# Kernel tuning notes

Measured on AMD Instinct MI355X. Metric: run time of the kernel, lower is better.

Reference implementation:

```python
import jax, jax.numpy as jnp
import numpy as np
from jax import lax

NUM_TAGS = 48
BATCH = 512
SEQ_LEN = 1024


def setup_inputs() -> dict:
    key = jax.random.key(0)
    k1, k2, k3, k4 = jax.random.split(key, 4)
    emissions = jax.random.normal(k1, (BATCH, SEQ_LEN, NUM_TAGS), dtype=jnp.float32)
    mask = jnp.ones((BATCH, SEQ_LEN), dtype=jnp.int32)
    transitions = jax.random.normal(k2, (NUM_TAGS, NUM_TAGS), dtype=jnp.float32)
    start_transitions = jax.random.normal(k3, (NUM_TAGS,), dtype=jnp.float32)
    end_transitions = jax.random.normal(k4, (NUM_TAGS,), dtype=jnp.float32)
    return {
        "emissions": emissions,
        "mask": mask,
        "transitions": transitions,
        "start_transitions": start_transitions,
        "end_transitions": end_transitions,
    }


def reference(emissions, mask, transitions, start_transitions, end_transitions):
    """Viterbi decode. mask is accepted but unused, matching the original module."""
    # emissions: [B, S, T]
    init_scores = start_transitions + emissions[:, 0]  # [B, T]

    def step(scores, em_t):
        # scores: [B, T] best score ending in each prev tag
        scores_with_trans = scores[:, :, None] + transitions  # [B, Tprev, Tcur]
        idx = jnp.argmax(scores_with_trans, axis=1)            # [B, T] backpointers
        new_scores = jnp.max(scores_with_trans, axis=1) + em_t  # [B, T]
        return new_scores, idx

    # scan over timesteps 1..S-1 (time-major emissions)
    em_rest = jnp.swapaxes(emissions[:, 1:], 0, 1)  # [S-1, B, T]
    scores, backptrs = lax.scan(step, init_scores, em_rest)  # backptrs: [S-1, B, T]

    scores = scores + end_transitions
    best_tags = jnp.argmax(scores, axis=1)  # [B] tag at position S-1

    def backtrace(tag, bp_t):
        # tag: [B] tag at position t+1; bp_t: [B, T] backpointers into position t
        prev = jnp.take_along_axis(bp_t, tag[:, None], axis=1)[:, 0]
        return prev, tag  # emit tag at position t+1

    first_tag, tags_rest = lax.scan(backtrace, best_tags, backptrs, reverse=True)
    # tags_rest[i] = tag at position i+1, shape [S-1, B]
    best_paths = jnp.concatenate(
        [first_tag[:, None], jnp.swapaxes(tags_rest, 0, 1)], axis=1
    )  # [B, S]
    return best_paths
```

## Files before the change

kernel.cpp:

```cpp
#include <hip/hip_runtime.h>

#define NTAG 48
#define SEQ 1024
#define NBATCH 512

__device__ __forceinline__ float rl_f32(float v, int lane) {
    return __int_as_float(__builtin_amdgcn_readlane(__float_as_int(v), lane));
}

__device__ __forceinline__ float max3(float a, float b, float c) {
    float d;
    asm("v_max3_f32 %0, %1, %2, %3" : "=v"(d) : "v"(a), "v"(b), "v"(c));
    return d;
}

__global__ __launch_bounds__(64, 1) void crf_viterbi_kernel(
    const float* __restrict__ em,
    const float* __restrict__ trans,
    const float* __restrict__ start,
    const float* __restrict__ endt,
    int* __restrict__ out,
    unsigned char* __restrict__ bp)
{
    const int b  = blockIdx.x;
    const int j  = threadIdx.x;
    const int jj = (j < NTAG) ? j : (NTAG - 1);

    __shared__ int obuf[SEQ];

    float trg[NTAG];
#pragma unroll
    for (int i = 0; i < NTAG; ++i) trg[i] = trans[i * NTAG + jj];

    const float* emb = em + (size_t)b * SEQ * NTAG;
    unsigned char* bpb = bp + (size_t)b * SEQ * NTAG;

    float score = start[jj] + emb[jj];

    float em_p1 = emb[1 * NTAG + jj];
    float em_p2 = emb[2 * NTAG + jj];

    for (int t = 1; t < SEQ; ++t) {
        float em_j = em_p1;
        em_p1 = em_p2;
        int tn = (t + 2 < SEQ) ? (t + 2) : (SEQ - 1);
        em_p2 = emb[tn * NTAG + jj];

        float cand[NTAG];
#pragma unroll
        for (int i = 0; i < NTAG; ++i)
            cand[i] = rl_f32(score, i) + trg[i];

        float l1[16];
#pragma unroll
        for (int k = 0; k < 16; ++k)
            l1[k] = max3(cand[3 * k], cand[3 * k + 1], cand[3 * k + 2]);
        float l2[6];
#pragma unroll
        for (int k = 0; k < 5; ++k)
            l2[k] = max3(l1[3 * k], l1[3 * k + 1], l1[3 * k + 2]);
        l2[5] = l1[15];
        float m0 = max3(l2[0], l2[1], l2[2]);
        float m1 = max3(l2[3], l2[4], l2[5]);
        float best = fmaxf(m0, m1);

        int pi = 0;
#pragma unroll
        for (int i = NTAG - 1; i >= 0; --i)
            pi = (cand[i] == best) ? i : pi;

        if (j < NTAG) bpb[(size_t)t * NTAG + j] = (unsigned char)pi;
        score = best + em_j;
    }

    score += endt[jj];

    float m = rl_f32(score, 0); int tag = 0;
#pragma unroll
    for (int i = 1; i < NTAG; ++i) {
        float v = rl_f32(score, i);
        if (v > m) { m = v; tag = i; }
    }

    if (j == 0) obuf[SEQ - 1] = tag;

    int cur[16], nxt[16];
    int t = SEQ - 1;
    int n = 16;
#pragma unroll
    for (int k = 0; k < 16; ++k)
        cur[k] = (int)bpb[(size_t)(t - k) * NTAG + jj];

    while (t >= 1) {
        int t2 = t - n;
        int n2 = 0;
        if (t2 >= 1) {
            n2 = (t2 >= 16) ? 16 : t2;
#pragma unroll
            for (int k = 0; k < 16; ++k)
                if (k < n2) nxt[k] = (int)bpb[(size_t)(t2 - k) * NTAG + jj];
        }
#pragma unroll
        for (int k = 0; k < 16; ++k) {
            if (k < n) {
                tag = __shfl(cur[k], tag, 64);
                if (j == 0) obuf[t - k - 1] = tag;
            }
        }
#pragma unroll
        for (int k = 0; k < 16; ++k) cur[k] = nxt[k];
        t = t2; n = n2;
    }

    __syncthreads();

    int* outb = out + (size_t)b * SEQ;
#pragma unroll
    for (int t0 = 0; t0 < SEQ / 64; ++t0)
        outb[t0 * 64 + j] = obuf[t0 * 64 + j];
}

extern "C" void kernel_launch(void* const* d_in, const int* in_sizes, int n_in,
                              void* d_out, int out_size, void* d_ws, size_t ws_size,
                              hipStream_t stream) {
    const float* em    = (const float*)d_in[0];
    const float* trans = (const float*)d_in[2];
    const float* start = (const float*)d_in[3];
    const float* endt  = (const float*)d_in[4];
    int* out = (int*)d_out;
    unsigned char* bpw = (unsigned char*)d_ws;

    crf_viterbi_kernel<<<NBATCH, 64, 0, stream>>>(em, trans, start, endt, out, bpw);
}
```

Baseline: 920.5 us.

## Store forward scores and recompute backpointers during backtrace instead of storing argmax

The forward Viterbi loop no longer computes or stores per-step argmax backpointers. Instead it writes each step's score row to workspace as floats. The backtrace recomputes the argmax from the stored scores plus a transposed transition matrix in LDS, using a wave max reduction and ballot. This removes the 48 compare/select ops per step from the serial forward chain. In exchange it quadruples workspace traffic and lengthens each serial backtrace step with several dependent shuffles.

Result: slower. 973.4 us (+5.7%).

```diff
diff --git a/kernel.cpp b/kernel.cpp
--- a/kernel.cpp
+++ b/kernel.cpp
@@ -3,6 +3,7 @@
 #define NTAG 48
 #define SEQ 1024
 #define NBATCH 512
+#define NEG_INF (-3.402823466e+38f)
 
 __device__ __forceinline__ float rl_f32(float v, int lane) {
     return __int_as_float(__builtin_amdgcn_readlane(__float_as_int(v), lane));
@@ -20,22 +21,33 @@
     const float* __restrict__ start,
     const float* __restrict__ endt,
     int* __restrict__ out,
-    unsigned char* __restrict__ bp)
+    float* __restrict__ srows)
 {
     const int b  = blockIdx.x;
     const int j  = threadIdx.x;
     const int jj = (j < NTAG) ? j : (NTAG - 1);
 
+    __shared__ float Ttr[NTAG * NTAG];
     __shared__ int obuf[SEQ];
+
+#pragma unroll
+    for (int k = 0; k < (NTAG * NTAG + 63) / 64; ++k) {
+        int idx = k * 64 + j;
+        if (idx < NTAG * NTAG) {
+            int i = idx / NTAG, c = idx % NTAG;
+            Ttr[c * NTAG + i] = trans[idx];
+        }
+    }
 
     float trg[NTAG];
 #pragma unroll
     for (int i = 0; i < NTAG; ++i) trg[i] = trans[i * NTAG + jj];
 
     const float* emb = em + (size_t)b * SEQ * NTAG;
-    unsigned char* bpb = bp + (size_t)b * SEQ * NTAG;
+    float* srb = srows + (size_t)b * SEQ * NTAG;
 
     float score = start[jj] + emb[jj];
+    if (j < NTAG) srb[j] = score;
 
     float em_p1 = emb[1 * NTAG + jj];
     float em_p2 = emb[2 * NTAG + jj];
@@ -46,70 +58,77 @@
         int tn = (t + 2 < SEQ) ? (t + 2) : (SEQ - 1);
         em_p2 = emb[tn * NTAG + jj];
 
-        float cand[NTAG];
-#pragma unroll
-        for (int i = 0; i < NTAG; ++i)
-            cand[i] = rl_f32(score, i) + trg[i];
-
         float l1[16];
 #pragma unroll
-        for (int k = 0; k < 16; ++k)
-            l1[k] = max3(cand[3 * k], cand[3 * k + 1], cand[3 * k + 2]);
+        for (int k = 0; k < 16; ++k) {
+            float c0 = rl_f32(score, 3 * k)     + trg[3 * k];
+            float c1 = rl_f32(score, 3 * k + 1) + trg[3 * k + 1];
+            float c2 = rl_f32(score, 3 * k + 2) + trg[3 * k + 2];
+            l1[k] = max3(c0, c1, c2);
+        }
         float l2[6];
-#pragma unroll
-        for (int k = 0; k < 5; ++k)
-            l2[k] = max3(l1[3 * k], l1[3 * k + 1], l1[3 * k + 2]);
+        l2[0] = max3(l1[0],  l1[1],  l1[2]);
+        l2[1] = max3(l1[3],  l1[4],  l1[5]);
+        l2[2] = max3(l1[6],  l1[7],  l1[8]);
+        l2[3] = max3(l1[9],  l1[10], l1[11]);
+        l2[4] = max3(l1[12], l1[13], l1[14]);
         l2[5] = l1[15];
         float m0 = max3(l2[0], l2[1], l2[2]);
         float m1 = max3(l2[3], l2[4], l2[5]);
         float best = fmaxf(m0, m1);
 
-        int pi = 0;
-#pragma unroll
-        for (int i = NTAG - 1; i >= 0; --i)
-            pi = (cand[i] == best) ? i : pi;
-
-        if (j < NTAG) bpb[(size_t)t * NTAG + j] = (unsigned char)pi;
         score = best + em_j;
+        if (j < NTAG) srb[(size_t)t * NTAG + j] = score;
     }
 
-    score += endt[jj];
+    float fs = (j < NTAG) ? (score + endt[jj]) : NEG_INF;
+    float mx = fs;
+    mx = fmaxf(mx, __shfl_xor(mx, 32, 64));
+    mx = fmaxf(mx, __shfl_xor(mx, 16, 64));
+    mx = fmaxf(mx, __shfl_xor(mx,  8, 64));
+    mx = fmaxf(mx, __shfl_xor(mx,  4, 64));
+    mx = fmaxf(mx, __shfl_xor(mx,  2, 64));
+    mx = fmaxf(mx, __shfl_xor(mx,  1, 64));
+    unsigned long long bl = __ballot(fs == mx);
+    int jt = __ffsll(bl) - 1;
 
-    float m = rl_f32(score, 0); int tag = 0;
+    if (j == 0) obuf[SEQ - 1] = jt;
+    __syncthreads();
+
+    float cur[8], nxt[8];
+    int r = SEQ - 2;
 #pragma unroll
-    for (int i = 1; i < NTAG; ++i) {
-        float v = rl_f32(score, i);
-        if (v > m) { m = v; tag = i; }
-    }
+    for (int k = 0; k < 8; ++k)
+        cur[k] = srb[(size_t)(r - k) * NTAG + jj];
 
-    if (j == 0) obuf[SEQ - 1] = tag;
+    int t = SEQ - 1;
+    while (t >= 1) {
+        int n = (t >= 8) ? 8 : t;
+        int r2 = r - 8;
+#pragma unroll
+        for (int k = 0; k < 8; ++k)
+            if (r2 - k >= 0) nxt[k] = srb[(size_t)(r2 - k) * NTAG + jj];
 
-    int cur[16], nxt[16];
-    int t = SEQ - 1;
-    int n = 16;
 #pragma unroll
-    for (int k = 0; k < 16; ++k)
-        cur[k] = (int)bpb[(size_t)(t - k) * NTAG + jj];
-
-    while (t >= 1) {
-        int t2 = t - n;
-        int n2 = 0;
-        if (t2 >= 1) {
-            n2 = (t2 >= 16) ? 16 : t2;
-#pragma unroll
-            for (int k = 0; k < 16; ++k)
-                if (k < n2) nxt[k] = (int)bpb[(size_t)(t2 - k) * NTAG + jj];
-        }
-#pragma unroll
-        for (int k = 0; k < 16; ++k) {
+        for (int k = 0; k < 8; ++k) {
             if (k < n) {
-                tag = __shfl(cur[k], tag, 64);
-                if (j == 0) obuf[t - k - 1] = tag;
+                float tv = Ttr[jt * NTAG + jj];
+                float v  = (j < NTAG) ? (cur[k] + tv) : NEG_INF;
+                float m  = v;
+                m = fmaxf(m, __shfl_xor(m, 32, 64));
+                m = fmaxf(m, __shfl_xor(m, 16, 64));
+                m = fmaxf(m, __shfl_xor(m,  8, 64));
+                m = fmaxf(m, __shfl_xor(m,  4, 64));
+                m = fmaxf(m, __shfl_xor(m,  2, 64));
+                m = fmaxf(m, __shfl_xor(m,  1, 64));
+                unsigned long long b2 = __ballot(v == m);
+                jt = __ffsll(b2) - 1;
+                if (j == 0) obuf[t - 1 - k] = jt;
             }
         }
+        t -= n; r -= 8;
 #pragma unroll
-        for (int k = 0; k < 16; ++k) cur[k] = nxt[k];
-        t = t2; n = n2;
+        for (int k = 0; k < 8; ++k) cur[k] = nxt[k];
     }
 
     __syncthreads();
@@ -128,7 +147,7 @@
     const float* start = (const float*)d_in[3];
     const float* endt  = (const float*)d_in[4];
     int* out = (int*)d_out;
-    unsigned char* bpw = (unsigned char*)d_ws;
+    float* srows = (float*)d_ws;
 
-    crf_viterbi_kernel<<<NBATCH, 64, 0, stream>>>(em, trans, start, endt, out, bpw);
+    crf_viterbi_kernel<<<NBATCH, 64, 0, stream>>>(em, trans, start, endt, out, srows);
 }
```
